# Kernel tuning notes

Measured on AMD Instinct MI355X. Metric: run time of the kernel, lower is better.

Reference implementation:

```python
import jax, jax.numpy as jnp
import numpy as np

B, N, D = 4, 2048, 1024


def setup_inputs() -> dict:
    key = jax.random.key(0)
    ks = jax.random.split(key, 9)
    x = jax.random.normal(ks[0], (B, N, D), dtype=jnp.float32)
    # causal mask: True = masked (set to -inf), per dot_product_attention semantics
    mask = jnp.triu(jnp.ones((N, N), dtype=bool), k=1)
    mask = jnp.broadcast_to(mask, (B, N, N))
    scale = 1.0 / np.sqrt(D)
    Wq = jax.random.normal(ks[1], (D, D), dtype=jnp.float32) * scale
    Wk = jax.random.normal(ks[2], (D, D), dtype=jnp.float32) * scale
    Wv = jax.random.normal(ks[3], (D, D), dtype=jnp.float32) * scale
    Wo = jax.random.normal(ks[4], (D, D), dtype=jnp.float32) * scale
    bq = jnp.zeros((D,), dtype=jnp.float32)
    bk = jnp.zeros((D,), dtype=jnp.float32)
    bv = jnp.zeros((D,), dtype=jnp.float32)
    bo = jnp.zeros((D,), dtype=jnp.float32)
    return {"x": x, "mask": mask, "Wq": Wq, "bq": bq, "Wk": Wk, "bk": bk,
            "Wv": Wv, "bv": bv, "Wo": Wo, "bo": bo}


def reference(x, mask, Wq, bq, Wk, bk, Wv, bv, Wo, bo):
    # QKV projections (single-head despite docstring; module never splits heads)
    Q = x @ Wq + bq  # [b, n, d]
    K = x @ Wk + bk
    V = x @ Wv + bv
    d = K.shape[-1]
    scores = jnp.einsum('bqd,bkd->bqk', Q, K) / jnp.sqrt(jnp.asarray(d, Q.dtype))
    min_infty = jnp.finfo(scores.dtype).min
    scores = jnp.where(mask, min_infty, scores)
    weights = jax.nn.softmax(scores, axis=-1)
    attention = jnp.einsum('bqk,bkd->bqd', weights, V)
    out = attention @ Wo + bo
    return out
```

## Files before the change

### kernel.cpp

```cpp
#include <hip/hip_runtime.h>
#include <hip/hip_bf16.h>

typedef __attribute__((ext_vector_type(8))) short short8;
typedef __attribute__((ext_vector_type(4))) float f32x4;

__device__ inline float b2f(unsigned short u) {
    union { unsigned int i; float f; } c; c.i = ((unsigned int)u) << 16; return c.f;
}
__device__ inline unsigned short f2b(float f) {
    __hip_bfloat16 h = __float2bfloat16(f);
    return *reinterpret_cast<unsigned short*>(&h);
}

__device__ inline void gl_lds16(const unsigned short* g, unsigned short* ldsbase) {
    __builtin_amdgcn_global_load_lds(
        (const __attribute__((address_space(1))) unsigned int*)(g),
        (__attribute__((address_space(3))) unsigned int*)(ldsbase),
        16, 0, 0);
}

__global__ __launch_bounds__(256) void prep(
    const float* __restrict__ x,
    const float* __restrict__ Wq, const float* __restrict__ Wk,
    const float* __restrict__ Wo, const float* __restrict__ Wv,
    const float* __restrict__ bv, const float* __restrict__ bo,
    unsigned short* __restrict__ xb,
    unsigned short* __restrict__ Wqt, unsigned short* __restrict__ Wkt,
    unsigned short* __restrict__ Wot, unsigned short* __restrict__ Wvb,
    float* __restrict__ bvo)
{
    const int z = blockIdx.z;
    const int t = threadIdx.x;
    __shared__ float tile[32][33];

    if (z < 3) {
        const float* src = z == 0 ? Wq : z == 1 ? Wk : Wo;
        unsigned short* dst = z == 0 ? Wqt : z == 1 ? Wkt : Wot;
        const int c0 = blockIdx.x * 32, r0 = blockIdx.y * 32;
        const int tx = t & 31, ty = t >> 5;
        #pragma unroll
        for (int i = ty; i < 32; i += 8)
            tile[i][tx] = src[(long)(r0 + i) * 1024 + c0 + tx];
        __syncthreads();
        #pragma unroll
        for (int i = ty; i < 32; i += 8)
            dst[(long)(c0 + i) * 1024 + r0 + tx] = f2b(tile[tx][i]);
        return;
    }
    if (z == 3) {
        const int i = (blockIdx.y * 32 + blockIdx.x) * 256 + t;
        float4 v = ((const float4*)Wv)[i];
        union { unsigned short u[4]; unsigned long long ll; } p;
        p.u[0] = f2b(v.x); p.u[1] = f2b(v.y); p.u[2] = f2b(v.z); p.u[3] = f2b(v.w);
        ((unsigned long long*)Wvb)[i] = p.ll;
        return;
    }
    if (z < 6) {
        const int bl = (z - 4) * 1024 + blockIdx.y * 32 + blockIdx.x;
        #pragma unroll
        for (int k = 0; k < 4; k++) {
            const int i = bl * 1024 + k * 256 + t;
            float4 v = ((const float4*)x)[i];
            union { unsigned short u[4]; unsigned long long ll; } p;
            p.u[0] = f2b(v.x); p.u[1] = f2b(v.y); p.u[2] = f2b(v.z); p.u[3] = f2b(v.w);
            ((unsigned long long*)xb)[i] = p.ll;
        }
        return;
    }
    if (blockIdx.y != 0) return;
    const int tx = t & 31, ty = t >> 5;
    const int n = blockIdx.x * 32 + tx;
    float acc = 0.f;
    #pragma unroll 4
    for (int j = 0; j < 128; j++) {
        const int k = ty * 128 + j;
        acc += Wo[(long)k * 1024 + n] * bv[k];
    }
    float* red = &tile[0][0];
    red[ty * 32 + tx] = acc;
    __syncthreads();
    if (ty == 0) {
        float s = 0.f;
        #pragma unroll
        for (int j = 0; j < 8; j++) s += red[j * 32 + tx];
        bvo[n] = s + bo[n];
    }
}

#define TILE_KLOOP(As, Bs, gA, lda, gB, ldb, Keff) \
    for (int k0 = 0; k0 < (Keff); k0 += 64) { \
        _Pragma("unroll") for (int p = 0; p < 2; p++) \
            _Pragma("unroll") for (int h = 0; h < 2; h++) { \
                gl_lds16((gA) + (long)h * 16 * (lda) + k0 + p * 32, \
                         &(As)[p * 4096 + (w * 32 + h * 16) * 32]); \
                gl_lds16((gB) + (long)h * 16 * (ldb) + k0 + p * 32, \
                         &(Bs)[p * 4096 + (w * 32 + h * 16) * 32]); \
            } \
        __syncthreads(); \
        _Pragma("unroll") for (int p = 0; p < 2; p++) { \
            short8 af[4], bfr[4]; \
            _Pragma("unroll") for (int mi = 0; mi < 4; mi++) \
                af[mi] = *(const short8*)&(As)[p * 4096 + (wr * 64 + mi * 16 + lrow) * 32 + quad * 8]; \
            _Pragma("unroll") for (int ni = 0; ni < 4; ni++) \
                bfr[ni] = *(const short8*)&(Bs)[p * 4096 + (wc * 64 + ni * 16 + lrow) * 32 + quad * 8]; \
            _Pragma("unroll") for (int mi = 0; mi < 4; mi++) \
                _Pragma("unroll") for (int ni = 0; ni < 4; ni++) \
                    acc[mi][ni] = __builtin_amdgcn_mfma_f32_16x16x32_bf16( \
                        af[mi], bfr[ni], acc[mi][ni], 0, 0, 0); \
        } \
        __syncthreads(); \
    }

#define TILE_DECLS \
    const int t = threadIdx.x, lane = t & 63, w = t >> 6; \
    const int wr = w >> 1, wc = w & 1; \
    const int lrow = lane & 15, quad = lane >> 4; \
    f32x4 acc[4][4]; \
    _Pragma("unroll") for (int i = 0; i < 4; i++) \
        _Pragma("unroll") for (int j = 0; j < 4; j++) \
            acc[i][j] = (f32x4){0.f, 0.f, 0.f, 0.f};

template<bool TRI, bool KCAUSAL, int OMODE>
__global__ __launch_bounds__(256) void gemm128(
    const unsigned short* __restrict__ A, const unsigned short* __restrict__ Bt,
    const float* __restrict__ bias, void* __restrict__ Cv,
    int K, int lda, int ldb, int ldc, long sA, long sB, long sC, float scale)
{
    __shared__ __attribute__((aligned(16))) unsigned short As[2 * 128 * 32];
    __shared__ __attribute__((aligned(16))) unsigned short Bs[2 * 128 * 32];
    int bm, bn, bz;
    if (TRI) {
        const int q = gridDim.x - 1 - blockIdx.x;
        bm = (int)((sqrtf(8.f * q + 1.f) - 1.f) * 0.5f);
        while ((bm + 1) * (bm + 2) / 2 <= q) bm++;
        while (bm * (bm + 1) / 2 > q) bm--;
        bn = q - bm * (bm + 1) / 2;
        bz = blockIdx.y;
    } else {
        bm = KCAUSAL ? (gridDim.x - 1 - blockIdx.x) : blockIdx.x;
        bn = blockIdx.y; bz = blockIdx.z;
    }
    A  += (long)bz * sA;
    Bt += (long)bz * sB;
    const int m0 = bm * 128, n0 = bn * 128;

    TILE_DECLS

    const int Keff = KCAUSAL ? ((bm + 1) * 128 < K ? (bm + 1) * 128 : K) : K;
    const unsigned short* gA = A  + (long)(m0 + w * 32 + (lane >> 2)) * lda + (lane & 3) * 8;
    const unsigned short* gB = Bt + (long)(n0 + w * 32 + (lane >> 2)) * ldb + (lane & 3) * 8;
    TILE_KLOOP(As, Bs, gA, lda, gB, ldb, Keff)

    #pragma unroll
    for (int mi = 0; mi < 4; mi++) {
        const int m = m0 + wr * 64 + mi * 16 + quad * 4;
        #pragma unroll
        for (int ni = 0; ni < 4; ni++) {
            const int n = n0 + wc * 64 + ni * 16 + lrow;
            const float bvl = bias ? bias[n] : 0.f;
            #pragma unroll
            for (int rg = 0; rg < 4; rg++) {
                const float val = acc[mi][ni][rg] * scale + bvl;
                if (OMODE == 1)
                    ((float*)Cv)[(long)bz * sC + (long)(m + rg) * ldc + n] = val;
                else
                    ((unsigned short*)Cv)[(long)bz * sC + (long)(m + rg) * ldc + n] = f2b(val);
            }
        }
    }
}

__global__ __launch_bounds__(256, 2) void qkv_proj(
    const unsigned short* __restrict__ A,
    const unsigned short* __restrict__ Wqt, const unsigned short* __restrict__ Wkt,
    const unsigned short* __restrict__ Wvot,
    const float* __restrict__ bq, const float* __restrict__ bk,
    unsigned short* __restrict__ Q, unsigned short* __restrict__ Km,
    unsigned short* __restrict__ Vot)
{
    __shared__ __attribute__((aligned(16))) unsigned short smem[32768];
    unsigned short* As  = smem;
    unsigned short* Bs0 = smem + 8192;
    unsigned short* Bs1 = smem + 16384;
    unsigned short* Bs2 = smem + 24576;
    unsigned short* pool = smem;

    const int bid = blockIdx.x;
    const int bnn = bid & 7, bm = bid >> 3;
    const int m0 = bm * 128, n0 = bnn * 128;

    const int t = threadIdx.x, lane = t & 63, w = t >> 6;
    const int wr = w >> 1, wc = w & 1;
    const int lrow = lane & 15, quad = lane >> 4;

    f32x4 accQ[4][4], accK[4][4], accV[4][4];
    #pragma unroll
    for (int i = 0; i < 4; i++)
        #pragma unroll
        for (int j = 0; j < 4; j++) {
            accQ[i][j] = (f32x4){0.f, 0.f, 0.f, 0.f};
            accK[i][j] = (f32x4){0.f, 0.f, 0.f, 0.f};
            accV[i][j] = (f32x4){0.f, 0.f, 0.f, 0.f};
        }

    const long rowA = (long)(m0 + w * 32 + (lane >> 2)) * 1024 + (lane & 3) * 8;
    const long rowB = (long)(n0 + w * 32 + (lane >> 2)) * 1024 + (lane & 3) * 8;
    const unsigned short* gA  = A    + rowA;
    const unsigned short* gB0 = Wqt  + rowB;
    const unsigned short* gB1 = Wkt  + rowB;
    const unsigned short* gB2 = Wvot + rowB;

    for (int k0 = 0; k0 < 1024; k0 += 64) {
        #pragma unroll
        for (int p = 0; p < 2; p++)
            #pragma unroll
            for (int h = 0; h < 2; h++) {
                const int ldst = p * 4096 + (w * 32 + h * 16) * 32;
                const long gofs = (long)h * 16 * 1024 + k0 + p * 32;
                gl_lds16(gA  + gofs, &As[ldst]);
                gl_lds16(gB0 + gofs, &Bs0[ldst]);
                gl_lds16(gB1 + gofs, &Bs1[ldst]);
                gl_lds16(gB2 + gofs, &Bs2[ldst]);
            }
        __syncthreads();
        #pragma unroll
        for (int p = 0; p < 2; p++) {
            short8 af[4], bfr[4];
            #pragma unroll
            for (int mi = 0; mi < 4; mi++)
                af[mi] = *(const short8*)&As[p * 4096 + (wr * 64 + mi * 16 + lrow) * 32 + quad * 8];
            #pragma unroll
            for (int ni = 0; ni < 4; ni++)
                bfr[ni] = *(const short8*)&Bs0[p * 4096 + (wc * 64 + ni * 16 + lrow) * 32 + quad * 8];
            #pragma unroll
            for (int mi = 0; mi < 4; mi++)
                #pragma unroll
                for (int ni = 0; ni < 4; ni++)
                    accQ[mi][ni] = __builtin_amdgcn_mfma_f32_16x16x32_bf16(
                        af[mi], bfr[ni], accQ[mi][ni], 0, 0, 0);
            #pragma unroll
            for (int ni = 0; ni < 4; ni++)
                bfr[ni] = *(const short8*)&Bs1[p * 4096 + (wc * 64 + ni * 16 + lrow) * 32 + quad * 8];
            #pragma unroll
            for (int mi = 0; mi < 4; mi++)
                #pragma unroll
                for (int ni = 0; ni < 4; ni++)
                    accK[mi][ni] = __builtin_amdgcn_mfma_f32_16x16x32_bf16(
                        af[mi], bfr[ni], accK[mi][ni], 0, 0, 0);
            #pragma unroll
            for (int ni = 0; ni < 4; ni++)
                bfr[ni] = *(const short8*)&Bs2[p * 4096 + (wc * 64 + ni * 16 + lrow) * 32 + quad * 8];
            #pragma unroll
            for (int mi = 0; mi < 4; mi++)
                #pragma unroll
                for (int ni = 0; ni < 4; ni++)
                    accV[mi][ni] = __builtin_amdgcn_mfma_f32_16x16x32_bf16(
                        af[mi], bfr[ni], accV[mi][ni], 0, 0, 0);
        }
        __syncthreads();
    }

    #pragma unroll
    for (int mi = 0; mi < 4; mi++)
        #pragma unroll
        for (int ni = 0; ni < 4; ni++) {
            const int n_l = wc * 64 + ni * 16 + lrow;
            const float bvl = bq[n0 + n_l];
            #pragma unroll
            for (int rg = 0; rg < 4; rg++) {
                const int m_l = wr * 64 + mi * 16 + quad * 4 + rg;
                pool[m_l * 128 + n_l] = f2b(accQ[mi][ni][rg] + bvl);
            }
        }
    __syncthreads();
    #pragma unroll
    for (int it = 0; it < 8; it++) {
        const int idx = it * 256 + t;
        const int m_l = idx >> 4, c = idx & 15;
        short8 v = *(const short8*)&pool[m_l * 128 + c * 8];
        *(short8*)&Q[(long)(m0 + m_l) * 1024 + n0 + c * 8] = v;
    }
    __syncthreads();

    #pragma unroll
    for (int mi = 0; mi < 4; mi++)
        #pragma unroll
        for (int ni = 0; ni < 4; ni++) {
            const int n_l = wc * 64 + ni * 16 + lrow;
            const float bvl = bk[n0 + n_l];
            #pragma unroll
            for (int rg = 0; rg < 4; rg++) {
                const int m_l = wr * 64 + mi * 16 + quad * 4 + rg;
                pool[m_l * 128 + n_l] = f2b(accK[mi][ni][rg] + bvl);
            }
        }
    __syncthreads();
    #pragma unroll
    for (int it = 0; it < 8; it++) {
        const int idx = it * 256 + t;
        const int m_l = idx >> 4, c = idx & 15;
        short8 v = *(const short8*)&pool[m_l * 128 + c * 8];
        *(short8*)&Km[(long)(m0 + m_l) * 1024 + n0 + c * 8] = v;
    }
    __syncthreads();

    #pragma unroll
    for (int mi = 0; mi < 4; mi++)
        #pragma unroll
        for (int ni = 0; ni < 4; ni++) {
            const int n_l = wc * 64 + ni * 16 + lrow;
            const int mb = wr * 64 + mi * 16 + quad * 4;
            union { unsigned short u[4]; unsigned long long ll; } pk;
            #pragma unroll
            for (int rg = 0; rg < 4; rg++) pk.u[rg] = f2b(accV[mi][ni][rg]);
            *(unsigned long long*)&pool[n_l * 128 + (mb ^ ((n_l & 15) << 3))] = pk.ll;
        }
    __syncthreads();
    #pragma unroll
    for (int it = 0; it < 8; it++) {
        const int idx = it * 256 + t;
        const int n_l = idx >> 4, c = idx & 15;
        short8 v = *(const short8*)&pool[n_l * 128 + ((c * 8) ^ ((n_l & 15) << 3))];
        *(short8*)&Vot[(long)(n0 + n_l) * 8192 + m0 + c * 8] = v;
    }
}

__global__ __launch_bounds__(256) void softmax_causal(unsigned short* __restrict__ S)
{
    const int i = blockIdx.x;
    const int t = threadIdx.x;
    const int padded = ((i >> 7) + 1) << 7;
    const int j0 = t * 8;
    const bool active = j0 < padded;

    __shared__ float red[4];

    for (int b = 0; b < 4; b++) {
        unsigned short* base = S + ((long)b * 2048 + i) * 2048;

        float v[8];
        if (active) {
            short8 s8 = *(const short8*)(base + j0);
            #pragma unroll
            for (int jj = 0; jj < 8; jj++)
                v[jj] = (j0 + jj <= i) ? b2f((unsigned short)s8[jj]) : -3.0e38f;
        } else {
            #pragma unroll
            for (int jj = 0; jj < 8; jj++) v[jj] = -3.0e38f;
        }

        float lmax = v[0];
        #pragma unroll
        for (int jj = 1; jj < 8; jj++) lmax = fmaxf(lmax, v[jj]);
        #pragma unroll
        for (int off = 32; off > 0; off >>= 1) lmax = fmaxf(lmax, __shfl_xor(lmax, off, 64));
        if ((t & 63) == 0) red[t >> 6] = lmax;
        __syncthreads();
        const float gmax = fmaxf(fmaxf(red[0], red[1]), fmaxf(red[2], red[3]));
        __syncthreads();

        float lsum = 0.f;
        #pragma unroll
        for (int jj = 0; jj < 8; jj++) {
            v[jj] = (v[jj] > -1.0e37f) ? __expf(v[jj] - gmax) : 0.f;
            lsum += v[jj];
        }
        #pragma unroll
        for (int off = 32; off > 0; off >>= 1) lsum += __shfl_xor(lsum, off, 64);
        if ((t & 63) == 0) red[t >> 6] = lsum;
        __syncthreads();
        const float inv = 1.0f / (red[0] + red[1] + red[2] + red[3]);

        if (active) {
            short8 p8;
            #pragma unroll
            for (int jj = 0; jj < 8; jj++) p8[jj] = (short)f2b(v[jj] * inv);
            *(short8*)(base + j0) = p8;
        }
        __syncthreads();
    }
}

extern "C" void kernel_launch(void* const* d_in, const int* in_sizes, int n_in,
                              void* d_out, int out_size, void* d_ws, size_t ws_size,
                              hipStream_t stream)
{
    const float* x  = (const float*)d_in[0];
    const float* Wq = (const float*)d_in[2];
    const float* bq = (const float*)d_in[3];
    const float* Wk = (const float*)d_in[4];
    const float* bk = (const float*)d_in[5];
    const float* Wv = (const float*)d_in[6];
    const float* bv = (const float*)d_in[7];
    const float* Wo = (const float*)d_in[8];
    const float* bo = (const float*)d_in[9];

    unsigned short* ws = (unsigned short*)d_ws;
    const long XSZ = 8192L * 1024;
    const long WSZ = 1024L * 1024;
    unsigned short* xb   = ws;
    unsigned short* Wqt  = ws + XSZ;
    unsigned short* Wkt  = Wqt + WSZ;
    unsigned short* Wot  = Wkt + WSZ;
    unsigned short* Wvb  = Wot + WSZ;
    unsigned short* Wvot = Wvb + WSZ;
    unsigned short* Q    = Wvot + WSZ;
    unsigned short* Km   = Q + XSZ;
    unsigned short* Vot  = Km + XSZ;
    unsigned short* S    = Vot + XSZ;
    float*          bvo  = (float*)(S + 4L * 2048 * 2048);

    const dim3 blk(256);

    prep<<<dim3(32, 32, 7), blk, 0, stream>>>(
        x, Wq, Wk, Wo, Wv, bv, bo, xb, Wqt, Wkt, Wot, Wvb, bvo);

    gemm128<false, false, 0><<<dim3(8, 8, 1), blk, 0, stream>>>(
        Wot, Wvb, nullptr, Wvot, 1024, 1024, 1024, 1024, 0, 0, 0, 1.f);

    qkv_proj<<<dim3(512), blk, 0, stream>>>(
        xb, Wqt, Wkt, Wvot, bq, bk, Q, Km, Vot);

    gemm128<true, false, 0><<<dim3(136, 4), blk, 0, stream>>>(
        Q, Km, nullptr, S, 1024, 1024, 1024, 2048,
        2048L * 1024, 2048L * 1024, 2048L * 2048, 0.03125f);

    softmax_causal<<<dim3(2048), blk, 0, stream>>>(S);

    gemm128<false, true, 1><<<dim3(16, 8, 4), blk, 0, stream>>>(
        S, Vot, bvo, (float*)d_out, 2048, 2048, 8192, 1024,
        2048L * 2048, 2048, 2048L * 1024, 1.f);
}
```

Measured before the change: 334.1 us.

## Use 128x256 tiles for QK^T and PV GEMMs with shared A tile

Replaces the generic templated gemm128 used for the causal score and PV products with dedicated kernels that compute a 128x256 output tile per block. Each block reuses one A tile against two B tiles, halving A traffic per output and doubling MFMA work per LDS sync. The triangular block mapping is rewritten for 256-wide column pairs. The cost is twice the accumulator registers and more LDS per block, which may reduce occupancy. The triangular tiling is also coarser, so some masked work may be computed that was skipped before.

```diff
diff --git a/kernel.cpp b/kernel.cpp
--- a/kernel.cpp
+++ b/kernel.cpp
@@ -120,36 +120,19 @@
         _Pragma("unroll") for (int j = 0; j < 4; j++) \
             acc[i][j] = (f32x4){0.f, 0.f, 0.f, 0.f};
 
-template<bool TRI, bool KCAUSAL, int OMODE>
 __global__ __launch_bounds__(256) void gemm128(
     const unsigned short* __restrict__ A, const unsigned short* __restrict__ Bt,
-    const float* __restrict__ bias, void* __restrict__ Cv,
-    int K, int lda, int ldb, int ldc, long sA, long sB, long sC, float scale)
+    unsigned short* __restrict__ C)
 {
     __shared__ __attribute__((aligned(16))) unsigned short As[2 * 128 * 32];
     __shared__ __attribute__((aligned(16))) unsigned short Bs[2 * 128 * 32];
-    int bm, bn, bz;
-    if (TRI) {
-        const int q = gridDim.x - 1 - blockIdx.x;
-        bm = (int)((sqrtf(8.f * q + 1.f) - 1.f) * 0.5f);
-        while ((bm + 1) * (bm + 2) / 2 <= q) bm++;
-        while (bm * (bm + 1) / 2 > q) bm--;
-        bn = q - bm * (bm + 1) / 2;
-        bz = blockIdx.y;
-    } else {
-        bm = KCAUSAL ? (gridDim.x - 1 - blockIdx.x) : blockIdx.x;
-        bn = blockIdx.y; bz = blockIdx.z;
-    }
-    A  += (long)bz * sA;
-    Bt += (long)bz * sB;
-    const int m0 = bm * 128, n0 = bn * 128;
+    const int m0 = blockIdx.x * 128, n0 = blockIdx.y * 128;
 
     TILE_DECLS
 
-    const int Keff = KCAUSAL ? ((bm + 1) * 128 < K ? (bm + 1) * 128 : K) : K;
-    const unsigned short* gA = A  + (long)(m0 + w * 32 + (lane >> 2)) * lda + (lane & 3) * 8;
-    const unsigned short* gB = Bt + (long)(n0 + w * 32 + (lane >> 2)) * ldb + (lane & 3) * 8;
-    TILE_KLOOP(As, Bs, gA, lda, gB, ldb, Keff)
+    const unsigned short* gA = A  + (long)(m0 + w * 32 + (lane >> 2)) * 1024 + (lane & 3) * 8;
+    const unsigned short* gB = Bt + (long)(n0 + w * 32 + (lane >> 2)) * 1024 + (lane & 3) * 8;
+    TILE_KLOOP(As, Bs, gA, 1024, gB, 1024, 1024)
 
     #pragma unroll
     for (int mi = 0; mi < 4; mi++) {
@@ -157,14 +140,134 @@
         #pragma unroll
         for (int ni = 0; ni < 4; ni++) {
             const int n = n0 + wc * 64 + ni * 16 + lrow;
-            const float bvl = bias ? bias[n] : 0.f;
+            #pragma unroll
+            for (int rg = 0; rg < 4; rg++)
+                C[(long)(m + rg) * 1024 + n] = f2b(acc[mi][ni][rg]);
+        }
+    }
+}
+
+#define TILE2_DECLS \
+    const int t = threadIdx.x, lane = t & 63, w = t >> 6; \
+    const int wr = w >> 1, wc = w & 1; \
+    const int lrow = lane & 15, quad = lane >> 4; \
+    f32x4 acc0[4][4], acc1[4][4]; \
+    _Pragma("unroll") for (int i = 0; i < 4; i++) \
+        _Pragma("unroll") for (int j = 0; j < 4; j++) { \
+            acc0[i][j] = (f32x4){0.f, 0.f, 0.f, 0.f}; \
+            acc1[i][j] = (f32x4){0.f, 0.f, 0.f, 0.f}; \
+        }
+
+#define TILE2_KLOOP(gA, lda, gB0, gB1, ldb, Keff) \
+    for (int k0 = 0; k0 < (Keff); k0 += 64) { \
+        _Pragma("unroll") for (int p = 0; p < 2; p++) \
+            _Pragma("unroll") for (int h = 0; h < 2; h++) { \
+                const int ldst = p * 4096 + (w * 32 + h * 16) * 32; \
+                const long gofs = (long)h * 16 * (lda) + k0 + p * 32; \
+                const long gofsB = (long)h * 16 * (ldb) + k0 + p * 32; \
+                gl_lds16((gA)  + gofs,  &As[ldst]); \
+                gl_lds16((gB0) + gofsB, &Bs0[ldst]); \
+                gl_lds16((gB1) + gofsB, &Bs1[ldst]); \
+            } \
+        __syncthreads(); \
+        _Pragma("unroll") for (int p = 0; p < 2; p++) { \
+            short8 af[4], bfr[4]; \
+            _Pragma("unroll") for (int mi = 0; mi < 4; mi++) \
+                af[mi] = *(const short8*)&As[p * 4096 + (wr * 64 + mi * 16 + lrow) * 32 + quad * 8]; \
+            _Pragma("unroll") for (int ni = 0; ni < 4; ni++) \
+                bfr[ni] = *(const short8*)&Bs0[p * 4096 + (wc * 64 + ni * 16 + lrow) * 32 + quad * 8]; \
+            _Pragma("unroll") for (int mi = 0; mi < 4; mi++) \
+                _Pragma("unroll") for (int ni = 0; ni < 4; ni++) \
+                    acc0[mi][ni] = __builtin_amdgcn_mfma_f32_16x16x32_bf16( \
+                        af[mi], bfr[ni], acc0[mi][ni], 0, 0, 0); \
+            _Pragma("unroll") for (int ni = 0; ni < 4; ni++) \
+                bfr[ni] = *(const short8*)&Bs1[p * 4096 + (wc * 64 + ni * 16 + lrow) * 32 + quad * 8]; \
+            _Pragma("unroll") for (int mi = 0; mi < 4; mi++) \
+                _Pragma("unroll") for (int ni = 0; ni < 4; ni++) \
+                    acc1[mi][ni] = __builtin_amdgcn_mfma_f32_16x16x32_bf16( \
+                        af[mi], bfr[ni], acc1[mi][ni], 0, 0, 0); \
+        } \
+        __syncthreads(); \
+    }
+
+__global__ __launch_bounds__(256, 2) void gemm_qk2(
+    const unsigned short* __restrict__ Q, const unsigned short* __restrict__ Km,
+    unsigned short* __restrict__ S)
+{
+    __shared__ __attribute__((aligned(16))) unsigned short As[8192];
+    __shared__ __attribute__((aligned(16))) unsigned short Bs0[8192];
+    __shared__ __attribute__((aligned(16))) unsigned short Bs1[8192];
+
+    const int q = 71 - blockIdx.x;
+    int tq = (int)sqrtf((float)q);
+    while (tq * tq + tq > q) tq--;
+    while ((tq + 1) * (tq + 1) + (tq + 1) <= q) tq++;
+    int bm, bp;
+    if (q >= (tq + 1) * (tq + 1)) { bm = 2 * tq + 1; bp = q - (tq + 1) * (tq + 1); }
+    else                          { bm = 2 * tq;     bp = q - (tq * tq + tq); }
+    const int bz = blockIdx.y;
+    const unsigned short* A  = Q  + (long)bz * 2048 * 1024;
+    const unsigned short* Bt = Km + (long)bz * 2048 * 1024;
+    const int m0 = bm * 128, n0 = bp * 256;
+
+    TILE2_DECLS
+
+    const unsigned short* gA  = A  + (long)(m0 + w * 32 + (lane >> 2)) * 1024 + (lane & 3) * 8;
+    const unsigned short* gB0 = Bt + (long)(n0 + w * 32 + (lane >> 2)) * 1024 + (lane & 3) * 8;
+    const unsigned short* gB1 = gB0 + 128L * 1024;
+    TILE2_KLOOP(gA, 1024, gB0, gB1, 1024, 1024)
+
+    unsigned short* Sb = S + (long)bz * 2048 * 2048;
+    #pragma unroll
+    for (int mi = 0; mi < 4; mi++) {
+        const int m = m0 + wr * 64 + mi * 16 + quad * 4;
+        #pragma unroll
+        for (int ni = 0; ni < 4; ni++) {
+            const int nl = wc * 64 + ni * 16 + lrow;
             #pragma unroll
             for (int rg = 0; rg < 4; rg++) {
-                const float val = acc[mi][ni][rg] * scale + bvl;
-                if (OMODE == 1)
-                    ((float*)Cv)[(long)bz * sC + (long)(m + rg) * ldc + n] = val;
-                else
-                    ((unsigned short*)Cv)[(long)bz * sC + (long)(m + rg) * ldc + n] = f2b(val);
+                Sb[(long)(m + rg) * 2048 + n0 + nl]       = f2b(acc0[mi][ni][rg] * 0.03125f);
+                Sb[(long)(m + rg) * 2048 + n0 + 128 + nl] = f2b(acc1[mi][ni][rg] * 0.03125f);
+            }
+        }
+    }
+}
+
+__global__ __launch_bounds__(256, 2) void gemm_pv2(
+    const unsigned short* __restrict__ S, const unsigned short* __restrict__ Vot,
+    const float* __restrict__ bvo, float* __restrict__ out)
+{
+    __shared__ __attribute__((aligned(16))) unsigned short As[8192];
+    __shared__ __attribute__((aligned(16))) unsigned short Bs0[8192];
+    __shared__ __attribute__((aligned(16))) unsigned short Bs1[8192];
+
+    const int bm = 15 - (int)blockIdx.x;
+    const int bn2 = blockIdx.y, bz = blockIdx.z;
+    const unsigned short* A  = S   + (long)bz * 2048 * 2048;
+    const unsigned short* Bt = Vot + (long)bz * 2048;
+    const int m0 = bm * 128, n0 = bn2 * 256;
+    const int Keff = (bm + 1) * 128;
+
+    TILE2_DECLS
+
+    const unsigned short* gA  = A  + (long)(m0 + w * 32 + (lane >> 2)) * 2048 + (lane & 3) * 8;
+    const unsigned short* gB0 = Bt + (long)(n0 + w * 32 + (lane >> 2)) * 8192 + (lane & 3) * 8;
+    const unsigned short* gB1 = gB0 + 128L * 8192;
+    TILE2_KLOOP(gA, 2048, gB0, gB1, 8192, Keff)
+
+    float* ob = out + (long)bz * 2048 * 1024;
+    #pragma unroll
+    for (int mi = 0; mi < 4; mi++) {
+        const int m = m0 + wr * 64 + mi * 16 + quad * 4;
+        #pragma unroll
+        for (int ni = 0; ni < 4; ni++) {
+            const int nl = wc * 64 + ni * 16 + lrow;
+            const float bv0 = bvo[n0 + nl];
+            const float bv1 = bvo[n0 + 128 + nl];
+            #pragma unroll
+            for (int rg = 0; rg < 4; rg++) {
+                ob[(long)(m + rg) * 1024 + n0 + nl]       = acc0[mi][ni][rg] + bv0;
+                ob[(long)(m + rg) * 1024 + n0 + 128 + nl] = acc1[mi][ni][rg] + bv1;
             }
         }
     }
@@ -415,19 +518,14 @@
     prep<<<dim3(32, 32, 7), blk, 0, stream>>>(
         x, Wq, Wk, Wo, Wv, bv, bo, xb, Wqt, Wkt, Wot, Wvb, bvo);
 
-    gemm128<false, false, 0><<<dim3(8, 8, 1), blk, 0, stream>>>(
-        Wot, Wvb, nullptr, Wvot, 1024, 1024, 1024, 1024, 0, 0, 0, 1.f);
+    gemm128<<<dim3(8, 8), blk, 0, stream>>>(Wot, Wvb, Wvot);
 
     qkv_proj<<<dim3(512), blk, 0, stream>>>(
         xb, Wqt, Wkt, Wvot, bq, bk, Q, Km, Vot);
 
-    gemm128<true, false, 0><<<dim3(136, 4), blk, 0, stream>>>(
-        Q, Km, nullptr, S, 1024, 1024, 1024, 2048,
-        2048L * 1024, 2048L * 1024, 2048L * 2048, 0.03125f);
+    gemm_qk2<<<dim3(72, 4), blk, 0, stream>>>(Q, Km, S);
 
     softmax_causal<<<dim3(2048), blk, 0, stream>>>(S);
 
-    gemm128<false, true, 1><<<dim3(16, 8, 4), blk, 0, stream>>>(
-        S, Vot, bvo, (float*)d_out, 2048, 2048, 8192, 1024,
-        2048L * 2048, 2048, 2048L * 1024, 1.f);
-}
+    gemm_pv2<<<dim3(16, 4, 4), blk, 0, stream>>>(S, Vot, bvo, (float*)d_out);
+}
```

New measurement: 326.9 us. -2.2%, faster.
